# Optimization experiments

Measured on AMD Instinct MI355X. Metric: run time of the kernel, lower is better.

The kernel has to match this reference:

```python
import jax, jax.numpy as jnp
import numpy as np

NUM_USERS = 100_000
NUM_ITEMS = 400_000
N = NUM_USERS + NUM_ITEMS  # total nodes in bipartite graph
EMB = 64
N_LAYERS = 3
NNZ = 10_000_000


def setup_inputs() -> dict:
    key = jax.random.key(0)
    k1, k2, k3, k4, k5 = jax.random.split(key, 5)
    user_embeddings = jax.random.normal(k1, (NUM_USERS, EMB), dtype=jnp.float32)
    item_embeddings = jax.random.normal(k2, (NUM_ITEMS, EMB), dtype=jnp.float32)
    adj_rows = jax.random.randint(k3, (NNZ,), 0, N, dtype=jnp.int32)
    adj_cols = jax.random.randint(k4, (NNZ,), 0, N, dtype=jnp.int32)
    # symmetric-normalized adjacency values are small positive floats
    adj_vals = jax.random.uniform(k5, (NNZ,), dtype=jnp.float32) * 0.1
    return {
        "user_embeddings": user_embeddings,
        "item_embeddings": item_embeddings,
        "adj_vals": adj_vals,
        "adj_rows": adj_rows,
        "adj_cols": adj_cols,
    }


def _spmm(vals, rows, cols, x):
    # out[r] = sum_{nz : rows[nz]==r} vals[nz] * x[cols[nz]]
    return jax.ops.segment_sum(vals[:, None] * x[cols], rows, num_segments=N)


def reference(user_embeddings, item_embeddings, adj_vals, adj_rows, adj_cols):
    ego = jnp.concatenate([user_embeddings, item_embeddings], axis=0)  # [N, EMB]
    acc = ego
    for _ in range(N_LAYERS):
        ego = _spmm(adj_vals, adj_rows, adj_cols, ego)
        acc = acc + ego
    all_emb = acc / jnp.asarray(N_LAYERS + 1, dtype=ego.dtype)  # layer-mean
    return all_emb[:NUM_USERS], all_emb[NUM_USERS:]
```

## Files before the change

kernel.cpp:

```cpp
#include <hip/hip_runtime.h>


#define NUSERS 100000
#define NNODES 500000
#define EMB 64
#define COLBITS 19
#define CMASK ((1u << COLBITS) - 1u)

#define SBBITS 9
#define SBROWS (1 << SBBITS)
#define SBMASK (SBROWS - 1)
#define NSB ((NNODES + SBROWS - 1) / SBROWS)
#define TILE 7168
#define P2_THREADS 512
#define P2_CAP 12800
#define P2_K 25
#define SLACK_PAIRS 262144

typedef unsigned long long ull;

__device__ __forceinline__ unsigned pk2(float lo, float hi) {
  unsigned a = __float_as_uint(lo);
  unsigned b = __float_as_uint(hi);
  a = (a + 0x7fffu + ((a >> 16) & 1u)) >> 16;
  b = (b + 0x7fffu + ((b >> 16) & 1u)) & 0xffff0000u;
  return (a & 0xffffu) | b;
}
__device__ __forceinline__ float blo(unsigned u) { return __uint_as_float(u << 16); }
__device__ __forceinline__ float bhi(unsigned u) { return __uint_as_float(u & 0xffff0000u); }


__global__ void scan_buckets(const int* __restrict__ counts,
                             int* __restrict__ bptr, int n, int nnz) {
  __shared__ int s[512];
  const int t = threadIdx.x;
  const int base = t * 8;
  int e[8];
  int tsum = 0;
#pragma unroll
  for (int j = 0; j < 8; ++j) {
    e[j] = (base + j < n) ? counts[base + j] : 0;
    tsum += e[j];
  }
  s[t] = tsum;
  __syncthreads();
  for (int off = 1; off < 512; off <<= 1) {
    int v = (t >= off) ? s[t - off] : 0;
    __syncthreads();
    s[t] += v;
    __syncthreads();
  }
  int run = s[t] - tsum;
#pragma unroll
  for (int j = 0; j < 8; ++j) {
    if (base + j < n) bptr[base + j] = run;
    run += e[j];
  }
  if (t == 511) bptr[n] = nnz;
}

__global__ __launch_bounds__(256) void tile_hist(const int* __restrict__ rows, int nnz,
                                                 int* __restrict__ cntmat) {
  __shared__ int h[NSB];
  const int t = threadIdx.x;
  const int tile0 = blockIdx.x * TILE;
  const int tileN = min(TILE, nnz - tile0);
  if (tileN <= 0) return;
  for (int i = t; i < NSB; i += 256) h[i] = 0;
  __syncthreads();
  for (int i = t; i < tileN; i += 256) atomicAdd(&h[rows[tile0 + i] >> SBBITS], 1);
  __syncthreads();
  int* row = cntmat + (size_t)blockIdx.x * NSB;
  for (int i = t; i < NSB; i += 256) row[i] = h[i];
}

__global__ void colsum(const int* __restrict__ A, int ntiles, int tchunk,
                       int* __restrict__ counts) {
  int sb = blockIdx.x * 256 + threadIdx.x;
  if (sb >= NSB) return;
  int t0 = blockIdx.y * tchunk;
  int t1 = min(t0 + tchunk, ntiles);
  int sum = 0;
  for (int t = t0; t < t1; ++t) sum += A[(size_t)t * NSB + sb];
  if (sum) atomicAdd(&counts[sb], sum);
}

__global__ void col_base(int* __restrict__ A, int ntiles,
                         const int* __restrict__ bptr) {
  int sb = blockIdx.x * 64 + threadIdx.x;
  if (sb >= NSB) return;
  int run = bptr[sb];
  int t = 0;
  if (ntiles >= 16) {
    int b0 = A[(size_t)0 * NSB + sb], b1 = A[(size_t)1 * NSB + sb];
    int b2 = A[(size_t)2 * NSB + sb], b3 = A[(size_t)3 * NSB + sb];
    int b4 = A[(size_t)4 * NSB + sb], b5 = A[(size_t)5 * NSB + sb];
    int b6 = A[(size_t)6 * NSB + sb], b7 = A[(size_t)7 * NSB + sb];
    for (; t + 16 <= ntiles; t += 8) {
      int n0 = A[(size_t)(t + 8) * NSB + sb],  n1 = A[(size_t)(t + 9) * NSB + sb];
      int n2 = A[(size_t)(t + 10) * NSB + sb], n3 = A[(size_t)(t + 11) * NSB + sb];
      int n4 = A[(size_t)(t + 12) * NSB + sb], n5 = A[(size_t)(t + 13) * NSB + sb];
      int n6 = A[(size_t)(t + 14) * NSB + sb], n7 = A[(size_t)(t + 15) * NSB + sb];
      A[(size_t)(t + 0) * NSB + sb] = run; run += b0;
      A[(size_t)(t + 1) * NSB + sb] = run; run += b1;
      A[(size_t)(t + 2) * NSB + sb] = run; run += b2;
      A[(size_t)(t + 3) * NSB + sb] = run; run += b3;
      A[(size_t)(t + 4) * NSB + sb] = run; run += b4;
      A[(size_t)(t + 5) * NSB + sb] = run; run += b5;
      A[(size_t)(t + 6) * NSB + sb] = run; run += b6;
      A[(size_t)(t + 7) * NSB + sb] = run; run += b7;
      b0 = n0; b1 = n1; b2 = n2; b3 = n3;
      b4 = n4; b5 = n5; b6 = n6; b7 = n7;
    }
    A[(size_t)(t + 0) * NSB + sb] = run; run += b0;
    A[(size_t)(t + 1) * NSB + sb] = run; run += b1;
    A[(size_t)(t + 2) * NSB + sb] = run; run += b2;
    A[(size_t)(t + 3) * NSB + sb] = run; run += b3;
    A[(size_t)(t + 4) * NSB + sb] = run; run += b4;
    A[(size_t)(t + 5) * NSB + sb] = run; run += b5;
    A[(size_t)(t + 6) * NSB + sb] = run; run += b6;
    A[(size_t)(t + 7) * NSB + sb] = run; run += b7;
    t += 8;
  }
  for (; t < ntiles; ++t) {
    size_t i = (size_t)t * NSB + sb;
    int c = A[i];
    A[i] = run;
    run += c;
  }
}

__global__ __launch_bounds__(256) void scatter_sb(
    const int* __restrict__ rows, const int* __restrict__ cols,
    const float* __restrict__ vals, int nnz,
    const int* __restrict__ basemat, ull* __restrict__ pairs) {
  __shared__ ull stg[TILE];
  __shared__ ushort sbid[TILE];
  __shared__ int cnt[NSB];
  __shared__ int start[NSB];
  __shared__ int ssc[256];
  const int t = threadIdx.x;
  const int tile0 = blockIdx.x * TILE;
  const int tileN = min(TILE, nnz - tile0);
  if (tileN <= 0) return;

  for (int i = t; i < NSB; i += 256) cnt[i] = 0;
  __syncthreads();

  int rr[TILE / 256];
#pragma unroll
  for (int k = 0; k < TILE / 256; ++k) {
    int idx = tile0 + t + k * 256;
    rr[k] = (idx < nnz) ? rows[idx] : -1;
    if (rr[k] >= 0) atomicAdd(&cnt[rr[k] >> SBBITS], 1);
  }
  __syncthreads();

  {
    int c[4];
    int tsum = 0;
#pragma unroll
    for (int j = 0; j < 4; ++j) {
      int i = t * 4 + j;
      c[j] = (i < NSB) ? cnt[i] : 0;
      tsum += c[j];
    }
    ssc[t] = tsum;
    __syncthreads();
    for (int off = 1; off < 256; off <<= 1) {
      int v = (t >= off) ? ssc[t - off] : 0;
      __syncthreads();
      ssc[t] += v;
      __syncthreads();
    }
    int run = ssc[t] - tsum;
#pragma unroll
    for (int j = 0; j < 4; ++j) {
      int i = t * 4 + j;
      if (i < NSB) start[i] = run;
      run += c[j];
    }
  }
  __syncthreads();
  for (int i = t; i < NSB; i += 256) cnt[i] = 0;
  __syncthreads();

#pragma unroll
  for (int k = 0; k < TILE / 256; ++k) {
    int idx = tile0 + t + k * 256;
    if (idx < nnz) {
      int r = rr[k];
      int sb = r >> SBBITS;
      unsigned key = ((unsigned)(r & SBMASK) << COLBITS) | (unsigned)cols[idx];
      ull p = ((ull)__float_as_uint(vals[idx]) << 32) | key;
      int j = start[sb] + atomicAdd(&cnt[sb], 1);
      stg[j] = p;
      sbid[j] = (ushort)sb;
    }
  }
  __syncthreads();

  const int* __restrict__ baserow = basemat + (size_t)blockIdx.x * NSB;
  for (int j = t; j < tileN; j += 256) {
    int sb = sbid[j];
    pairs[baserow[sb] + (j - start[sb])] = stg[j];
  }
}

__global__ __launch_bounds__(P2_THREADS) void finalize_sb(
    const int* __restrict__ bptr, ull* __restrict__ pairs,
    int* __restrict__ rs, int* __restrict__ re,
    int* __restrict__ ovf_alloc, int nnz) {
  __shared__ int hist[SBROWS];
  __shared__ int start[SBROWS];
  __shared__ int cur[SBROWS];
  __shared__ ull out[P2_CAP];
  __shared__ int ovf_base;
  const int b = blockIdx.x;
  const int t = threadIdx.x;
  const int s = bptr[b];
  const int n = bptr[b + 1] - s;
  const bool ovf = (n > P2_CAP);

  hist[t] = 0;
  ull* __restrict__ slack = pairs + nnz;
  if (ovf && t == 0) ovf_base = atomicAdd(ovf_alloc, n);
  __syncthreads();

  ull q[P2_K];
  if (!ovf) {
#pragma unroll
    for (int k = 0; k < P2_K; ++k) {
      int idx = t + k * P2_THREADS;
      if (idx < n) {
        q[k] = pairs[s + idx];
        atomicAdd(&hist[(unsigned)q[k] >> COLBITS], 1);
      }
    }
  } else {
    for (int j = t; j < n; j += P2_THREADS) slack[ovf_base + j] = pairs[s + j];
    __syncthreads();
    for (int j = t; j < n; j += P2_THREADS)
      atomicAdd(&hist[(unsigned)slack[ovf_base + j] >> COLBITS], 1);
  }
  __syncthreads();

  start[t] = hist[t];
  __syncthreads();
  for (int off = 1; off < SBROWS; off <<= 1) {
    int v = (t >= off) ? start[t - off] : 0;
    __syncthreads();
    start[t] += v;
    __syncthreads();
  }
  int excl = start[t] - hist[t];
  cur[t] = excl;

  int row = b * SBROWS + t;
  if (row < NNODES) {
    rs[row] = s + excl;
    re[row] = s + excl + hist[t];
  }
  __syncthreads();

  if (!ovf) {
#pragma unroll
    for (int k = 0; k < P2_K; ++k) {
      int idx = t + k * P2_THREADS;
      if (idx < n) {
        unsigned key = (unsigned)q[k];
        int pos = atomicAdd(&cur[key >> COLBITS], 1);
        out[pos] = ((q[k] >> 32) << 32) | (key & CMASK);
      }
    }
    __syncthreads();
    for (int j = t; j < n; j += P2_THREADS) pairs[s + j] = out[j];
  } else {
    for (int j = t; j < n; j += P2_THREADS) {
      ull p = slack[ovf_base + j];
      unsigned key = (unsigned)p;
      int pos = atomicAdd(&cur[key >> COLBITS], 1);
      pairs[s + pos] = ((p >> 32) << 32) | (key & CMASK);
    }
  }
}

__global__ void conv_e16(const float4* __restrict__ user4,
                         const float4* __restrict__ item4,
                         uint2* __restrict__ E) {
  const int n4 = NNODES * EMB / 4;
  const int u4 = NUSERS * EMB / 4;
  int i = blockIdx.x * blockDim.x + threadIdx.x;
  if (i >= n4) return;
  float4 a = (i < u4) ? user4[i] : item4[i - u4];
  E[i] = make_uint2(pk2(a.x, a.y), pk2(a.z, a.w));
}

template <bool FINAL>
__global__ __launch_bounds__(256) void spmm_bf16(
    const int* __restrict__ rs, const int* __restrict__ re,
    const ull* __restrict__ pq, const ushort* __restrict__ T,
    const ushort* __restrict__ E0bf,
    const float* __restrict__ user_emb, const float* __restrict__ item_emb,
    void* __restrict__ dest, float scale) {
  const int lane = threadIdx.x & 63;
  const int sub  = lane >> 3;
  const int l4   = lane & 7;
  const int wid  = (int)((blockIdx.x * blockDim.x + threadIdx.x) >> 6);
  const int r = wid * 8 + sub;
  if (r >= NNODES) return;
  const int s = rs[r];
  const int e = re[r];
  const uint4* __restrict__ T4 = (const uint4*)T;

  float4 aL0 = make_float4(0.f, 0.f, 0.f, 0.f);
  float4 aH0 = make_float4(0.f, 0.f, 0.f, 0.f);
  float4 aL1 = make_float4(0.f, 0.f, 0.f, 0.f);
  float4 aH1 = make_float4(0.f, 0.f, 0.f, 0.f);

  auto fma8 = [&](float4& L, float4& H, float v, uint4 z) {
    L.x = fmaf(v, blo(z.x), L.x); L.y = fmaf(v, bhi(z.x), L.y);
    L.z = fmaf(v, blo(z.y), L.z); L.w = fmaf(v, bhi(z.y), L.w);
    H.x = fmaf(v, blo(z.z), H.x); H.y = fmaf(v, bhi(z.z), H.y);
    H.z = fmaf(v, blo(z.w), H.z); H.w = fmaf(v, bhi(z.w), H.w);
  };

  int i = s;
  for (; i + 3 < e; i += 4) {
    ull q0 = __builtin_nontemporal_load(&pq[i + 0]);
    ull q1 = __builtin_nontemporal_load(&pq[i + 1]);
    ull q2 = __builtin_nontemporal_load(&pq[i + 2]);
    ull q3 = __builtin_nontemporal_load(&pq[i + 3]);
    uint4 z0 = T4[(size_t)(unsigned)q0 * 8 + l4];
    uint4 z1 = T4[(size_t)(unsigned)q1 * 8 + l4];
    uint4 z2 = T4[(size_t)(unsigned)q2 * 8 + l4];
    uint4 z3 = T4[(size_t)(unsigned)q3 * 8 + l4];
    float v0 = __uint_as_float((unsigned)(q0 >> 32));
    float v1 = __uint_as_float((unsigned)(q1 >> 32));
    float v2 = __uint_as_float((unsigned)(q2 >> 32));
    float v3 = __uint_as_float((unsigned)(q3 >> 32));
    fma8(aL0, aH0, v0, z0);
    fma8(aL1, aH1, v1, z1);
    fma8(aL0, aH0, v2, z2);
    fma8(aL1, aH1, v3, z3);
  }
  for (; i < e; ++i) {
    ull q = __builtin_nontemporal_load(&pq[i]);
    uint4 z = T4[(size_t)(unsigned)q * 8 + l4];
    float v = __uint_as_float((unsigned)(q >> 32));
    fma8(aL0, aH0, v, z);
  }

  float4 aL, aH;
  aL.x = aL0.x + aL1.x; aL.y = aL0.y + aL1.y;
  aL.z = aL0.z + aL1.z; aL.w = aL0.w + aL1.w;
  aH.x = aH0.x + aH1.x; aH.y = aH0.y + aH1.y;
  aH.z = aH0.z + aH1.z; aH.w = aH0.w + aH1.w;

  float e0, e1, e2, e3, e4, e5, e6, e7;
  if (FINAL) {
    const ull* e0p = (r < NUSERS)
        ? (const ull*)(user_emb + (size_t)r * EMB)
        : (const ull*)(item_emb + (size_t)(r - NUSERS) * EMB);
    ull eq0 = __builtin_nontemporal_load(&e0p[l4 * 4 + 0]);
    ull eq1 = __builtin_nontemporal_load(&e0p[l4 * 4 + 1]);
    ull eq2 = __builtin_nontemporal_load(&e0p[l4 * 4 + 2]);
    ull eq3 = __builtin_nontemporal_load(&e0p[l4 * 4 + 3]);
    e0 = __uint_as_float((unsigned)eq0); e1 = __uint_as_float((unsigned)(eq0 >> 32));
    e2 = __uint_as_float((unsigned)eq1); e3 = __uint_as_float((unsigned)(eq1 >> 32));
    e4 = __uint_as_float((unsigned)eq2); e5 = __uint_as_float((unsigned)(eq2 >> 32));
    e6 = __uint_as_float((unsigned)eq3); e7 = __uint_as_float((unsigned)(eq3 >> 32));
  } else {
    uint4 ue = ((const uint4*)E0bf)[(size_t)r * 8 + l4];
    e0 = blo(ue.x); e1 = bhi(ue.x);
    e2 = blo(ue.y); e3 = bhi(ue.y);
    e4 = blo(ue.z); e5 = bhi(ue.z);
    e6 = blo(ue.w); e7 = bhi(ue.w);
  }

  if (FINAL) {
    float4 oL, oH;
    oL.x = scale * (e0 + aL.x); oL.y = scale * (e1 + aL.y);
    oL.z = scale * (e2 + aL.z); oL.w = scale * (e3 + aL.w);
    oH.x = scale * (e4 + aH.x); oH.y = scale * (e5 + aH.y);
    oH.z = scale * (e6 + aH.z); oH.w = scale * (e7 + aH.w);
    float4* d4 = (float4*)dest;
    d4[(size_t)r * 16 + l4 * 2 + 0] = oL;
    d4[(size_t)r * 16 + l4 * 2 + 1] = oH;
  } else {
    uint4 ob;
    ob.x = pk2(e0 + aL.x, e1 + aL.y);
    ob.y = pk2(e2 + aL.z, e3 + aL.w);
    ob.z = pk2(e4 + aH.x, e5 + aH.y);
    ob.w = pk2(e6 + aH.z, e7 + aH.w);
    ((uint4*)dest)[(size_t)r * 8 + l4] = ob;
  }
}


__global__ void spmm_atomic(const float* __restrict__ vals,
                            const int* __restrict__ rows,
                            const int* __restrict__ cols,
                            const float* __restrict__ user_emb,
                            const float* __restrict__ item_emb,
                            const float* __restrict__ prev, int nnz,
                            float* __restrict__ y) {
  const int lane = threadIdx.x & 63;
  int wave = (int)((blockIdx.x * blockDim.x + threadIdx.x) >> 6);
  const int nwaves = (int)((gridDim.x * blockDim.x) >> 6);
  for (int nz = wave; nz < nnz; nz += nwaves) {
    float v = vals[nz];
    int r = rows[nz];
    int c = cols[nz];
    float xv = (c < NUSERS) ? user_emb[(size_t)c * EMB + lane]
                            : item_emb[(size_t)(c - NUSERS) * EMB + lane];
    if (prev) xv += prev[(size_t)c * EMB + lane];
    atomicAdd(&y[(size_t)r * EMB + lane], v * xv);
  }
}

__global__ void finalize_kernel(const float4* __restrict__ user4,
                                const float4* __restrict__ item4,
                                float4* __restrict__ X4) {
  const int n4 = NNODES * EMB / 4;
  const int u4 = NUSERS * EMB / 4;
  int i = blockIdx.x * blockDim.x + threadIdx.x;
  if (i >= n4) return;
  float4 a = (i < u4) ? user4[i] : item4[i - u4];
  float4 b = X4[i];
  b.x = 0.25f * (a.x + b.x);
  b.y = 0.25f * (a.y + b.y);
  b.z = 0.25f * (a.z + b.z);
  b.w = 0.25f * (a.w + b.w);
  X4[i] = b;
}


extern "C" void kernel_launch(void* const* d_in, const int* in_sizes, int n_in,
                              void* d_out, int out_size, void* d_ws, size_t ws_size,
                              hipStream_t stream) {
  const float* user_emb = (const float*)d_in[0];
  const float* item_emb = (const float*)d_in[1];
  const float* vals     = (const float*)d_in[2];
  const int*   rows     = (const int*)d_in[3];
  const int*   cols     = (const int*)d_in[4];
  const int nnz = in_sizes[2];
  float* W = (float*)d_out;

  const float4* user4 = (const float4*)user_emb;
  const float4* item4 = (const float4*)item_emb;

  const int ntiles = (nnz + TILE - 1) / TILE;

  const size_t bfBytes   = (size_t)NNODES * EMB * 2;
  const size_t embBytes  = (size_t)NNODES * EMB * sizeof(float);
  const size_t pairBytes = ((size_t)nnz + SLACK_PAIRS) * sizeof(ull);
  const size_t rsBytes   = ((size_t)NNODES * 4 + 255) & ~(size_t)255;
  const size_t reBytes   = rsBytes;
  const size_t ptrBytes  = ((size_t)(NSB + 1) * 4 + 255) & ~(size_t)255;
  const size_t cntBytes  = ((size_t)NSB * 4 + 255) & ~(size_t)255;
  const size_t matBytes  = (((size_t)ntiles * NSB * 4) + 255) & ~(size_t)255;
  const size_t ovfBytes  = 256;
  const size_t need = 2 * bfBytes + pairBytes + rsBytes + reBytes + ptrBytes +
                      cntBytes + matBytes + ovfBytes;

  dim3 blk(256);

  if (ws_size < need) {
    float* Y = (float*)d_ws;
    hipMemsetAsync(W, 0, embBytes, stream);
    hipMemsetAsync(Y, 0, embBytes, stream);
    dim3 grid(4096);
    spmm_atomic<<<grid, blk, 0, stream>>>(vals, rows, cols, user_emb, item_emb, nullptr, nnz, W);
    spmm_atomic<<<grid, blk, 0, stream>>>(vals, rows, cols, user_emb, item_emb, W, nnz, Y);
    hipMemsetAsync(W, 0, embBytes, stream);
    spmm_atomic<<<grid, blk, 0, stream>>>(vals, rows, cols, user_emb, item_emb, Y, nnz, W);
    const int n4 = NNODES * EMB / 4;
    finalize_kernel<<<(n4 + 255) / 256, blk, 0, stream>>>(user4, item4, (float4*)W);
    return;
  }

  char* ws = (char*)d_ws;
  ushort* bfA   = (ushort*)ws; ws += bfBytes;
  ushort* bfB   = (ushort*)ws; ws += bfBytes;
  ull*   pairs  = (ull*)ws;    ws += pairBytes;
  int*   rsArr  = (int*)ws;    ws += rsBytes;
  int*   reArr  = (int*)ws;    ws += reBytes;
  int*   bptr   = (int*)ws;    ws += ptrBytes;
  int*   counts = (int*)ws;    ws += cntBytes;
  int*   cntmat = (int*)ws;    ws += matBytes;
  int*   ovf    = (int*)ws;

  hipMemsetAsync(counts, 0, (size_t)NSB * 4, stream);
  hipMemsetAsync(ovf, 0, 4, stream);
  tile_hist<<<ntiles, blk, 0, stream>>>(rows, nnz, cntmat);
  {
    const int tchunk = (ntiles + 15) / 16;
    dim3 g((NSB + 255) / 256, 16);
    colsum<<<g, blk, 0, stream>>>(cntmat, ntiles, tchunk, counts);
  }
  scan_buckets<<<1, 512, 0, stream>>>(counts, bptr, NSB, nnz);
  col_base<<<(NSB + 63) / 64, 64, 0, stream>>>(cntmat, ntiles, bptr);
  scatter_sb<<<ntiles, blk, 0, stream>>>(rows, cols, vals, nnz, cntmat, pairs);
  finalize_sb<<<NSB, P2_THREADS, 0, stream>>>(bptr, pairs, rsArr, reArr, ovf, nnz);

  const int n4 = NNODES * EMB / 4;
  conv_e16<<<(n4 + 255) / 256, blk, 0, stream>>>(user4, item4, (uint2*)bfA);

  const int sgrid = NNODES / 32;
  spmm_bf16<false><<<sgrid, blk, 0, stream>>>(rsArr, reArr, pairs, bfA, bfA,
                                              user_emb, item_emb, bfB, 1.0f);
  spmm_bf16<false><<<sgrid, blk, 0, stream>>>(rsArr, reArr, pairs, bfB, bfA,
                                              user_emb, item_emb, bfA, 1.0f);
  spmm_bf16<true ><<<sgrid, blk, 0, stream>>>(rsArr, reArr, pairs, bfA, nullptr,
                                              user_emb, item_emb, W, 0.25f);
}
```

Before: 1.279 ms.

## Double super-block size, reuse tile histograms in scatter, drop LDS staging in finalize

Super-blocks grow from 512 to 1024 rows, which halves their number, and finalize now runs 1024 threads per block with 24 items each. col_base writes the base offsets into a separate matrix, so scatter_sb can read each tile's per-bucket counts from the precomputed count matrix instead of rebuilding the histogram with shared atomics. finalize_sb now writes each sorted pair straight to global memory instead of staging the block in shared memory and copying it out. This is meant to cut shared-memory use, atomics and barriers, at the cost of an extra workspace matrix and uncoalesced global writes in finalize.

```diff
diff --git a/kernel.cpp b/kernel.cpp
--- a/kernel.cpp
+++ b/kernel.cpp
@@ -7,14 +7,14 @@
 #define COLBITS 19
 #define CMASK ((1u << COLBITS) - 1u)
 
-#define SBBITS 9
+#define SBBITS 10
 #define SBROWS (1 << SBBITS)
 #define SBMASK (SBROWS - 1)
 #define NSB ((NNODES + SBROWS - 1) / SBROWS)
 #define TILE 7168
-#define P2_THREADS 512
-#define P2_CAP 12800
-#define P2_K 25
+#define P2_THREADS 1024
+#define P2_K 24
+#define P2_CAP (P2_THREADS * P2_K)
 #define SLACK_PAIRS 262144
 
 typedef unsigned long long ull;
@@ -85,47 +85,30 @@
   if (sum) atomicAdd(&counts[sb], sum);
 }
 
-__global__ void col_base(int* __restrict__ A, int ntiles,
-                         const int* __restrict__ bptr) {
+__global__ void col_base(const int* __restrict__ C, int* __restrict__ B,
+                         int ntiles, const int* __restrict__ bptr) {
   int sb = blockIdx.x * 64 + threadIdx.x;
   if (sb >= NSB) return;
   int run = bptr[sb];
   int t = 0;
-  if (ntiles >= 16) {
-    int b0 = A[(size_t)0 * NSB + sb], b1 = A[(size_t)1 * NSB + sb];
-    int b2 = A[(size_t)2 * NSB + sb], b3 = A[(size_t)3 * NSB + sb];
-    int b4 = A[(size_t)4 * NSB + sb], b5 = A[(size_t)5 * NSB + sb];
-    int b6 = A[(size_t)6 * NSB + sb], b7 = A[(size_t)7 * NSB + sb];
-    for (; t + 16 <= ntiles; t += 8) {
-      int n0 = A[(size_t)(t + 8) * NSB + sb],  n1 = A[(size_t)(t + 9) * NSB + sb];
-      int n2 = A[(size_t)(t + 10) * NSB + sb], n3 = A[(size_t)(t + 11) * NSB + sb];
-      int n4 = A[(size_t)(t + 12) * NSB + sb], n5 = A[(size_t)(t + 13) * NSB + sb];
-      int n6 = A[(size_t)(t + 14) * NSB + sb], n7 = A[(size_t)(t + 15) * NSB + sb];
-      A[(size_t)(t + 0) * NSB + sb] = run; run += b0;
-      A[(size_t)(t + 1) * NSB + sb] = run; run += b1;
-      A[(size_t)(t + 2) * NSB + sb] = run; run += b2;
-      A[(size_t)(t + 3) * NSB + sb] = run; run += b3;
-      A[(size_t)(t + 4) * NSB + sb] = run; run += b4;
-      A[(size_t)(t + 5) * NSB + sb] = run; run += b5;
-      A[(size_t)(t + 6) * NSB + sb] = run; run += b6;
-      A[(size_t)(t + 7) * NSB + sb] = run; run += b7;
-      b0 = n0; b1 = n1; b2 = n2; b3 = n3;
-      b4 = n4; b5 = n5; b6 = n6; b7 = n7;
-    }
-    A[(size_t)(t + 0) * NSB + sb] = run; run += b0;
-    A[(size_t)(t + 1) * NSB + sb] = run; run += b1;
-    A[(size_t)(t + 2) * NSB + sb] = run; run += b2;
-    A[(size_t)(t + 3) * NSB + sb] = run; run += b3;
-    A[(size_t)(t + 4) * NSB + sb] = run; run += b4;
-    A[(size_t)(t + 5) * NSB + sb] = run; run += b5;
-    A[(size_t)(t + 6) * NSB + sb] = run; run += b6;
-    A[(size_t)(t + 7) * NSB + sb] = run; run += b7;
-    t += 8;
+  for (; t + 8 <= ntiles; t += 8) {
+    int c0 = C[(size_t)(t + 0) * NSB + sb], c1 = C[(size_t)(t + 1) * NSB + sb];
+    int c2 = C[(size_t)(t + 2) * NSB + sb], c3 = C[(size_t)(t + 3) * NSB + sb];
+    int c4 = C[(size_t)(t + 4) * NSB + sb], c5 = C[(size_t)(t + 5) * NSB + sb];
+    int c6 = C[(size_t)(t + 6) * NSB + sb], c7 = C[(size_t)(t + 7) * NSB + sb];
+    B[(size_t)(t + 0) * NSB + sb] = run; run += c0;
+    B[(size_t)(t + 1) * NSB + sb] = run; run += c1;
+    B[(size_t)(t + 2) * NSB + sb] = run; run += c2;
+    B[(size_t)(t + 3) * NSB + sb] = run; run += c3;
+    B[(size_t)(t + 4) * NSB + sb] = run; run += c4;
+    B[(size_t)(t + 5) * NSB + sb] = run; run += c5;
+    B[(size_t)(t + 6) * NSB + sb] = run; run += c6;
+    B[(size_t)(t + 7) * NSB + sb] = run; run += c7;
   }
   for (; t < ntiles; ++t) {
     size_t i = (size_t)t * NSB + sb;
-    int c = A[i];
-    A[i] = run;
+    int c = C[i];
+    B[i] = run;
     run += c;
   }
 }
@@ -133,38 +116,26 @@
 __global__ __launch_bounds__(256) void scatter_sb(
     const int* __restrict__ rows, const int* __restrict__ cols,
     const float* __restrict__ vals, int nnz,
-    const int* __restrict__ basemat, ull* __restrict__ pairs) {
+    const int* __restrict__ cntmat, const int* __restrict__ basemat,
+    ull* __restrict__ pairs) {
   __shared__ ull stg[TILE];
   __shared__ ushort sbid[TILE];
-  __shared__ int cnt[NSB];
   __shared__ int start[NSB];
+  __shared__ int cur[NSB];
   __shared__ int ssc[256];
   const int t = threadIdx.x;
   const int tile0 = blockIdx.x * TILE;
   const int tileN = min(TILE, nnz - tile0);
   if (tileN <= 0) return;
 
-  for (int i = t; i < NSB; i += 256) cnt[i] = 0;
-  __syncthreads();
-
-  int rr[TILE / 256];
-#pragma unroll
-  for (int k = 0; k < TILE / 256; ++k) {
-    int idx = tile0 + t + k * 256;
-    rr[k] = (idx < nnz) ? rows[idx] : -1;
-    if (rr[k] >= 0) atomicAdd(&cnt[rr[k] >> SBBITS], 1);
-  }
-  __syncthreads();
+  const int* __restrict__ cntrow  = cntmat  + (size_t)blockIdx.x * NSB;
+  const int* __restrict__ baserow = basemat + (size_t)blockIdx.x * NSB;
 
   {
-    int c[4];
-    int tsum = 0;
-#pragma unroll
-    for (int j = 0; j < 4; ++j) {
-      int i = t * 4 + j;
-      c[j] = (i < NSB) ? cnt[i] : 0;
-      tsum += c[j];
-    }
+    const int i0 = 2 * t, i1 = 2 * t + 1;
+    int c0 = (i0 < NSB) ? cntrow[i0] : 0;
+    int c1 = (i1 < NSB) ? cntrow[i1] : 0;
+    int tsum = c0 + c1;
     ssc[t] = tsum;
     __syncthreads();
     for (int off = 1; off < 256; off <<= 1) {
@@ -173,34 +144,27 @@
       ssc[t] += v;
       __syncthreads();
     }
-    int run = ssc[t] - tsum;
-#pragma unroll
-    for (int j = 0; j < 4; ++j) {
-      int i = t * 4 + j;
-      if (i < NSB) start[i] = run;
-      run += c[j];
-    }
-  }
-  __syncthreads();
-  for (int i = t; i < NSB; i += 256) cnt[i] = 0;
+    int excl = ssc[t] - tsum;
+    if (i0 < NSB) { start[i0] = excl; cur[i0] = 0; }
+    if (i1 < NSB) { start[i1] = excl + c0; cur[i1] = 0; }
+  }
   __syncthreads();
 
 #pragma unroll
   for (int k = 0; k < TILE / 256; ++k) {
     int idx = tile0 + t + k * 256;
     if (idx < nnz) {
-      int r = rr[k];
+      int r = rows[idx];
       int sb = r >> SBBITS;
       unsigned key = ((unsigned)(r & SBMASK) << COLBITS) | (unsigned)cols[idx];
       ull p = ((ull)__float_as_uint(vals[idx]) << 32) | key;
-      int j = start[sb] + atomicAdd(&cnt[sb], 1);
+      int j = start[sb] + atomicAdd(&cur[sb], 1);
       stg[j] = p;
       sbid[j] = (ushort)sb;
     }
   }
   __syncthreads();
 
-  const int* __restrict__ baserow = basemat + (size_t)blockIdx.x * NSB;
   for (int j = t; j < tileN; j += 256) {
     int sb = sbid[j];
     pairs[baserow[sb] + (j - start[sb])] = stg[j];
@@ -214,7 +178,6 @@
   __shared__ int hist[SBROWS];
   __shared__ int start[SBROWS];
   __shared__ int cur[SBROWS];
-  __shared__ ull out[P2_CAP];
   __shared__ int ovf_base;
   const int b = blockIdx.x;
   const int t = threadIdx.x;
@@ -270,11 +233,9 @@
       if (idx < n) {
         unsigned key = (unsigned)q[k];
         int pos = atomicAdd(&cur[key >> COLBITS], 1);
-        out[pos] = ((q[k] >> 32) << 32) | (key & CMASK);
+        pairs[s + pos] = ((q[k] >> 32) << 32) | (key & CMASK);
       }
     }
-    __syncthreads();
-    for (int j = t; j < n; j += P2_THREADS) pairs[s + j] = out[j];
   } else {
     for (int j = t; j < n; j += P2_THREADS) {
       ull p = slack[ovf_base + j];
@@ -462,7 +423,7 @@
   const size_t matBytes  = (((size_t)ntiles * NSB * 4) + 255) & ~(size_t)255;
   const size_t ovfBytes  = 256;
   const size_t need = 2 * bfBytes + pairBytes + rsBytes + reBytes + ptrBytes +
-                      cntBytes + matBytes + ovfBytes;
+                      cntBytes + 2 * matBytes + ovfBytes;
 
   dim3 blk(256);
 
@@ -489,6 +450,7 @@
   int*   bptr   = (int*)ws;    ws += ptrBytes;
   int*   counts = (int*)ws;    ws += cntBytes;
   int*   cntmat = (int*)ws;    ws += matBytes;
+  int*   basemat= (int*)ws;    ws += matBytes;
   int*   ovf    = (int*)ws;
 
   hipMemsetAsync(counts, 0, (size_t)NSB * 4, stream);
@@ -500,8 +462,8 @@
     colsum<<<g, blk, 0, stream>>>(cntmat, ntiles, tchunk, counts);
   }
   scan_buckets<<<1, 512, 0, stream>>>(counts, bptr, NSB, nnz);
-  col_base<<<(NSB + 63) / 64, 64, 0, stream>>>(cntmat, ntiles, bptr);
-  scatter_sb<<<ntiles, blk, 0, stream>>>(rows, cols, vals, nnz, cntmat, pairs);
+  col_base<<<(NSB + 63) / 64, 64, 0, stream>>>(cntmat, basemat, ntiles, bptr);
+  scatter_sb<<<ntiles, blk, 0, stream>>>(rows, cols, vals, nnz, cntmat, basemat, pairs);
   finalize_sb<<<NSB, P2_THREADS, 0, stream>>>(bptr, pairs, rsArr, reArr, ovf, nnz);
 
   const int n4 = NNODES * EMB / 4;
```

Result: no change. 1.288 ms (+0.7%).
